# Kernel tuning notes

Hardware: AMD Instinct MI355X
Metric: run time of the kernel (lower is better)

Reference implementation:

```python
import jax, jax.numpy as jnp
import numpy as np

EPS = 1e-5
NUM_HEADS = 8
TOP_K = 4

def _ln(x, s, b):
    m = x.mean(-1, keepdims=True)
    v = ((x - m) ** 2).mean(-1, keepdims=True)
    return (x - m) / jnp.sqrt(v + EPS) * s + b

def _mha(x, wq, bq, wk, bk, wv, bv, wo, bo):
    B, S, D = x.shape
    dh = D // NUM_HEADS
    q = (x @ wq + bq).reshape(B, S, NUM_HEADS, dh)
    k = (x @ wk + bk).reshape(B, S, NUM_HEADS, dh)
    v = (x @ wv + bv).reshape(B, S, NUM_HEADS, dh)
    att = jnp.einsum('bqhd,bkhd->bhqk', q, k) / np.sqrt(dh).astype(x.dtype)
    a = jax.nn.softmax(att, axis=-1)
    o = jnp.einsum('bhqk,bkhd->bqhd', a, v).reshape(B, S, D)
    return o @ wo + bo

def _moe(x, rd, ru, w1, b1, w2, b2, ws1, bs1, ws2, bs2):
    B, S, D = x.shape
    N = B * S
    E = ru.shape[-1]
    t = x.reshape(N, D)
    scores = (t @ rd) @ ru                       # [N,E] low-rank router
    probs = jax.nn.softmax(scores, axis=-1)
    tv, ti = jax.lax.top_k(probs, TOP_K)          # [N,K]
    tw = tv / tv.sum(-1, keepdims=True)           # renormalized gate weights
    oh = jax.nn.one_hot(ti, E, dtype=t.dtype)     # [N,K,E]
    gates = (oh * tw[..., None]).sum(1)           # sparse [N,E] combine weights
    h = jax.nn.gelu(jnp.einsum('nd,edh->enh', t, w1) + b1[:, None, :])
    eo = jnp.einsum('enh,ehd->end', h, w2) + b2[:, None, :]
    routed = jnp.einsum('end,ne->nd', eo, gates)
    shared = jax.nn.gelu(t @ ws1 + bs1) @ ws2 + bs2
    out = (routed + shared).reshape(B, S, D)
    # aux losses: load-balance + router z-loss
    f = oh.sum(1).mean(0)                         # mean assignments per expert
    P = probs.mean(0)
    lb = (E / TOP_K) * jnp.sum(f * P)
    z = jnp.mean(jax.nn.logsumexp(scores, axis=-1) ** 2)
    return out, lb, z

def reference(x, ln1_s, ln1_b, ln2_s, ln2_b, wq, bq, wk, bk, wv, bv, wo, bo,
              router_down, router_up, w1, b1, w2, b2, ws1, bs1, ws2, bs2, fn_s, fn_b):
    L = wq.shape[0]
    lbs, zs = [], []
    for l in range(L):
        x = x + _mha(_ln(x, ln1_s[l], ln1_b[l]), wq[l], bq[l], wk[l], bk[l],
                     wv[l], bv[l], wo[l], bo[l])
        moe_out, lb, z = _moe(_ln(x, ln2_s[l], ln2_b[l]), router_down[l], router_up[l],
                              w1[l], b1[l], w2[l], b2[l], ws1[l], bs1[l], ws2[l], bs2[l])
        x = x + moe_out
        lbs.append(lb)
        zs.append(z)
    x = _ln(x, fn_s, fn_b)
    return x, jnp.stack(lbs), jnp.stack(zs)

def setup_inputs() -> dict:
    key = jax.random.key(0)
    ks = jax.random.split(key, 16)
    L, D, E, R, H, HS, B, S = 2, 512, 32, 64, 512, 4096, 4, 1024
    w = 0.02  # init scale for weights
    return {
        'x': jax.random.normal(ks[0], (B, S, D), jnp.float32),
        'ln1_s': jnp.ones((L, D)), 'ln1_b': jnp.zeros((L, D)),
        'ln2_s': jnp.ones((L, D)), 'ln2_b': jnp.zeros((L, D)),
        'wq': jax.random.normal(ks[1], (L, D, D)) * w, 'bq': jnp.zeros((L, D)),
        'wk': jax.random.normal(ks[2], (L, D, D)) * w, 'bk': jnp.zeros((L, D)),
        'wv': jax.random.normal(ks[3], (L, D, D)) * w, 'bv': jnp.zeros((L, D)),
        'wo': jax.random.normal(ks[4], (L, D, D)) * w, 'bo': jnp.zeros((L, D)),
        'router_down': jax.random.normal(ks[5], (L, D, R)) * w,
        'router_up': jax.random.normal(ks[6], (L, R, E)) * w,
        'w1': jax.random.normal(ks[7], (L, E, D, H)) * w, 'b1': jnp.zeros((L, E, H)),
        'w2': jax.random.normal(ks[8], (L, E, H, D)) * w, 'b2': jnp.zeros((L, E, D)),
        'ws1': jax.random.normal(ks[9], (L, D, HS)) * w, 'bs1': jnp.zeros((L, HS)),
        'ws2': jax.random.normal(ks[10], (L, HS, D)) * w, 'bs2': jnp.zeros((L, D)),
        'fn_s': jnp.ones((D,)), 'fn_b': jnp.zeros((D,)),
    }
```

## Files before the change

### kernel.cpp

```cpp
#include <hip/hip_runtime.h>
#include <math.h>

#define NTOK    4096
#define DMODEL  512
#define NEXP    32
#define RRANK   64
#define HEXP    512
#define HSHARED 4096
#define SEQ     1024
#define BATCH   4
#define NHEAD   8
#define TOPK    4
#define NLAYER  2
#define QBLK    64
#define KBLK    64
#define MAXTILE 160
#define DDU     262144

typedef __attribute__((ext_vector_type(8))) short bf16x8;
typedef __attribute__((ext_vector_type(4))) float f32x4;

__device__ __forceinline__ float gelu_f(float x) {
    float t = tanhf(0.7978845608028654f * (x + 0.044715f * x * x * x));
    return 0.5f * x * (1.f + t);
}
__device__ __forceinline__ unsigned short f2bf(float f) {
    unsigned int u = __float_as_uint(f);
    u += 0x7FFFu + ((u >> 16) & 1u);
    return (unsigned short)(u >> 16);
}
__device__ __forceinline__ float bf2f(unsigned short u) {
    return __uint_as_float((unsigned int)u << 16);
}
__device__ __forceinline__ void gl_lds16(const void* g, void* l) {
    __builtin_amdgcn_global_load_lds(
        (const __attribute__((address_space(1))) void*)g,
        (__attribute__((address_space(3))) void*)l, 16, 0, 0);
}

template <int MODE>
__global__ __launch_bounds__(256) void ln_kernel(const float* __restrict__ x,
                                                 const float* __restrict__ s,
                                                 const float* __restrict__ b,
                                                 float* __restrict__ outf,
                                                 unsigned short* __restrict__ outb) {
    int wave = threadIdx.x >> 6, lane = threadIdx.x & 63;
    int row = blockIdx.x * 4 + wave;
    const float* xr = x + (size_t)row * DMODEL;
    float v[8];
    float sum = 0.f;
#pragma unroll
    for (int i = 0; i < 8; i++) { v[i] = xr[lane + i * 64]; sum += v[i]; }
#pragma unroll
    for (int o = 32; o; o >>= 1) sum += __shfl_xor(sum, o);
    float m = sum * (1.f / DMODEL);
    float vs = 0.f;
#pragma unroll
    for (int i = 0; i < 8; i++) { float d = v[i] - m; vs += d * d; }
#pragma unroll
    for (int o = 32; o; o >>= 1) vs += __shfl_xor(vs, o);
    float rstd = rsqrtf(vs * (1.f / DMODEL) + 1e-5f);
#pragma unroll
    for (int i = 0; i < 8; i++) {
        int c = lane + i * 64;
        float r = (v[i] - m) * rstd * s[c] + b[c];
        if (MODE != 1) outf[(size_t)row * DMODEL + c] = r;
        if (MODE != 0) outb[(size_t)row * DMODEL + c] = f2bf(r);
    }
}

template <int SK, bool MOE, int MODE, bool ROUTER = false>
__global__ __launch_bounds__(256) void reduceln_kernel(
    const float* __restrict__ pbuf, const float* __restrict__ bias,
    const unsigned short* __restrict__ eogb, const float* __restrict__ topw,
    const int* __restrict__ pos, float* __restrict__ xb,
    const float* __restrict__ s, const float* __restrict__ b,
    float* __restrict__ outf, unsigned short* __restrict__ outb,
    const float* __restrict__ rdru, float* __restrict__ rsc) {
    int wave = threadIdx.x >> 6, lane = threadIdx.x & 63;
    int row = blockIdx.x * 4 + wave;
    int cb = lane * 8;
    size_t base = (size_t)row * DMODEL + cb;
    float v[8];
    {
        float4 a0 = *(const float4*)(xb + base);
        float4 a1 = *(const float4*)(xb + base + 4);
        float4 b0 = *(const float4*)(bias + cb);
        float4 b1 = *(const float4*)(bias + cb + 4);
        v[0] = a0.x + b0.x; v[1] = a0.y + b0.y; v[2] = a0.z + b0.z; v[3] = a0.w + b0.w;
        v[4] = a1.x + b1.x; v[5] = a1.y + b1.y; v[6] = a1.z + b1.z; v[7] = a1.w + b1.w;
    }
#pragma unroll
    for (int sk = 0; sk < SK; sk++) {
        const float* p = pbuf + (size_t)sk * NTOK * DMODEL + base;
        float4 p0 = *(const float4*)p;
        float4 p1 = *(const float4*)(p + 4);
        v[0] += p0.x; v[1] += p0.y; v[2] += p0.z; v[3] += p0.w;
        v[4] += p1.x; v[5] += p1.y; v[6] += p1.z; v[7] += p1.w;
    }
    if (MOE) {
#pragma unroll
        for (int k = 0; k < TOPK; k++) {
            float w = topw[row * TOPK + k];
            bf16x8 e = *(const bf16x8*)(eogb + (size_t)pos[row * TOPK + k] * DMODEL + cb);
#pragma unroll
            for (int i = 0; i < 8; i++) v[i] += w * bf2f((unsigned short)e[i]);
        }
    }
    *(float4*)(xb + base) = make_float4(v[0], v[1], v[2], v[3]);
    *(float4*)(xb + base + 4) = make_float4(v[4], v[5], v[6], v[7]);
    float sum = 0.f;
#pragma unroll
    for (int i = 0; i < 8; i++) sum += v[i];
#pragma unroll
    for (int o = 32; o; o >>= 1) sum += __shfl_xor(sum, o);
    float m = sum * (1.f / DMODEL);
    float vs = 0.f;
#pragma unroll
    for (int i = 0; i < 8; i++) { float d = v[i] - m; vs += d * d; }
#pragma unroll
    for (int o = 32; o; o >>= 1) vs += __shfl_xor(vs, o);
    float rstd = rsqrtf(vs * (1.f / DMODEL) + 1e-5f);
    float rr[8];
#pragma unroll
    for (int i = 0; i < 8; i++) {
        int c = cb + i;
        rr[i] = (v[i] - m) * rstd * s[c] + b[c];
        if (MODE != 1) outf[(size_t)row * DMODEL + c] = rr[i];
        if (MODE != 0) outb[(size_t)row * DMODEL + c] = f2bf(rr[i]);
    }
    if (ROUTER) {
        float sc[NEXP];
#pragma unroll
        for (int e = 0; e < NEXP; e++) sc[e] = 0.f;
#pragma unroll
        for (int i = 0; i < 8; i++) {
            const float4* rp = (const float4*)(rdru + (size_t)(cb + i) * NEXP);
            float rv = rr[i];
#pragma unroll
            for (int e4 = 0; e4 < 8; e4++) {
                float4 q = rp[e4];
                sc[e4 * 4 + 0] += rv * q.x;
                sc[e4 * 4 + 1] += rv * q.y;
                sc[e4 * 4 + 2] += rv * q.z;
                sc[e4 * 4 + 3] += rv * q.w;
            }
        }
#pragma unroll
        for (int e = 0; e < NEXP; e++) {
#pragma unroll
            for (int o = 32; o; o >>= 1) sc[e] += __shfl_xor(sc[e], o);
        }
        if (lane == 0) {
            float* rp = rsc + (size_t)row * NEXP;
#pragma unroll
            for (int e = 0; e < NEXP; e++) rp[e] = sc[e];
        }
    }
}

__global__ __launch_bounds__(256) void wtall_kernel(
    const float* __restrict__ wq, const float* __restrict__ wk,
    const float* __restrict__ wv, const float* __restrict__ wo,
    const float* __restrict__ w1, const float* __restrict__ w2,
    const float* __restrict__ ws1, const float* __restrict__ ws2,
    const float* __restrict__ bq, const float* __restrict__ bk, const float* __restrict__ bv,
    unsigned short* __restrict__ wqkvt, unsigned short* __restrict__ wot,
    unsigned short* __restrict__ w1t, unsigned short* __restrict__ w2t,
    unsigned short* __restrict__ ws1t, unsigned short* __restrict__ ws2t,
    float* __restrict__ bqkv, int* __restrict__ stats) {
    __shared__ float tbuf[64][68];
    int bkid = blockIdx.x;
    int tid = threadIdx.x;
    if (bkid >= 5376) {
        int i = (bkid - 5376) * 256 + tid;
        float val = (i < 512) ? bq[i] : (i < 1024 ? bk[i - 512] : bv[i - 1024]);
        bqkv[i] = val;
        if (i < 160) stats[i] = 0;
        return;
    }
    const float* src;
    unsigned short* dst;
    int K, N, tx, ty;
    if (bkid < 256) {
        int w = bkid >> 6, t = bkid & 63;
        K = 512; N = 512; ty = t >> 3; tx = t & 7;
        if (w == 0)      { src = wq; dst = wqkvt; }
        else if (w == 1) { src = wk; dst = wqkvt + DDU; }
        else if (w == 2) { src = wv; dst = wqkvt + 2 * (size_t)DDU; }
        else             { src = wo; dst = wot; }
    } else if (bkid < 2304) {
        int t = bkid - 256; int e = t >> 6; int tt = t & 63;
        K = 512; N = 512; ty = tt >> 3; tx = tt & 7;
        src = w1 + (size_t)e * DDU; dst = w1t + (size_t)e * DDU;
    } else if (bkid < 4352) {
        int t = bkid - 2304; int e = t >> 6; int tt = t & 63;
        K = 512; N = 512; ty = tt >> 3; tx = tt & 7;
        src = w2 + (size_t)e * DDU; dst = w2t + (size_t)e * DDU;
    } else if (bkid < 4864) {
        int t = bkid - 4352;
        K = 512; N = 4096; tx = t & 63; ty = t >> 6;
        src = ws1; dst = ws1t;
    } else {
        int t = bkid - 4864;
        K = 4096; N = 512; tx = t & 7; ty = t >> 3;
        src = ws2; dst = ws2t;
    }
    int k0 = ty * 64, n0 = tx * 64;
    int r = tid >> 2, cb4 = (tid & 3) * 4;
#pragma unroll
    for (int i = 0; i < 4; i++)
        *(float4*)&tbuf[r][cb4 + i * 16] = *(const float4*)(src + (size_t)(k0 + r) * N + n0 + cb4 + i * 16);
    __syncthreads();
    int g = tid & 7, nr = tid >> 3;
#pragma unroll
    for (int i = 0; i < 2; i++) {
        int n = nr + i * 32;
        bf16x8 v;
#pragma unroll
        for (int j = 0; j < 8; j++) v[j] = (short)f2bf(tbuf[g * 8 + j][n]);
        *(bf16x8*)(dst + (size_t)(n0 + n) * K + k0 + g * 8) = v;
    }
}

__global__ __launch_bounds__(256) void vtr_kernel(const unsigned short* __restrict__ QKV,
                                                  unsigned short* __restrict__ Vt) {
    int st = blockIdx.x, hh = blockIdx.y, bb = blockIdx.z;
    __shared__ unsigned short t[64][72];
    int r = threadIdx.x >> 3, g = threadIdx.x & 7;
#pragma unroll
    for (int i = 0; i < 2; i++) {
        int row = r + i * 32;
        bf16x8 v = *(const bf16x8*)(QKV + (size_t)(bb * SEQ + st * 64 + row) * 1536 + 1024 + hh * 64 + g * 8);
        *(bf16x8*)&t[row][g * 8] = v;
    }
    __syncthreads();
#pragma unroll
    for (int i = 0; i < 2; i++) {
        int d = r + i * 32;
        bf16x8 v;
#pragma unroll
        for (int j = 0; j < 8; j++) v[j] = (short)t[g * 8 + j][d];
        *(bf16x8*)(Vt + (size_t)((bb * NHEAD + hh) * 64 + d) * SEQ + st * 64 + g * 8) = v;
    }
}

template <bool GELU, bool GATHER, bool EXPERT, bool OUTBF16, int SK>
__device__ __forceinline__ void gemm_body(
    char* asb, char* bsb,
    unsigned int rb, unsigned int gx, unsigned int tot, int zidx,
    const unsigned short* Ab, const unsigned short* Wt,
    const float* bias, void* Cvoid, int M, int Nn, int Kk,
    const int* rowmap, const int* cntp, const int* offp, const int* tinfo) {
    constexpr int RS  = 128;
    constexpr int CH  = 8;
    constexpr int RPI = 8;
    constexpr int AIW = 4;
    constexpr int BIW = 2;
    unsigned int lg = (rb & 7) * (tot >> 3) + (rb >> 3);
    unsigned int bx = lg % gx;
    unsigned int by = lg / gx;
    int n0 = bx * 64;
    int m0;
    size_t cbase = 0;
    int kbeg = 0, kend = Kk;
    if (EXPERT) {
        int t = by;
        if (t >= tinfo[0]) return;
        int e = tinfo[1 + 2 * t];
        m0 = tinfo[2 + 2 * t];
        M = cntp[e];
        Wt += (size_t)e * Nn * Kk;
        bias += (size_t)e * Nn;
        int oe = offp[e];
        cbase = (size_t)oe * Nn;
        if (GATHER) rowmap += oe;
        else Ab += (size_t)oe * Kk;
    } else {
        m0 = by * 128;
    }
    if (SK > 1) {
        int chunk = Kk / SK;
        kbeg = zidx * chunk;
        kend = kbeg + chunk;
        cbase = (size_t)zidx * M * Nn;
    }
    int tid = threadIdx.x;
    int wave = tid >> 6, lane = tid & 63;
    int wm = wave >> 1, wn = wave & 1;
    int l15 = lane & 15, l16 = lane >> 4;
    int c16 = lane & (CH - 1);
    int ro  = lane / CH;

    const char* aptr[AIW];
    const char* bptr[BIW];
#pragma unroll
    for (int j = 0; j < AIW; j++) {
        int rloc = j * RPI + ro;
        int row = wave * 32 + rloc;
        int grow = m0 + row;
        int arow = GATHER ? rowmap[grow] : grow;
        int srcoff = ((c16 ^ (rloc & (CH - 1))) << 4);
        aptr[j] = (const char*)Ab + (((size_t)arow * Kk) << 1) + srcoff;
    }
#pragma unroll
    for (int j = 0; j < BIW; j++) {
        int rloc = j * RPI + ro;
        int row = wave * 16 + rloc;
        int srcoff = ((c16 ^ (rloc & (CH - 1))) << 4);
        bptr[j] = (const char*)Wt + (((size_t)(n0 + row) * Kk) << 1) + srcoff;
    }

    f32x4 acc[4][2];
#pragma unroll
    for (int m = 0; m < 4; m++)
#pragma unroll
        for (int n = 0; n < 2; n++)
#pragma unroll
            for (int j = 0; j < 4; j++) acc[m][n][j] = 0.f;

    for (int k0 = kbeg; k0 < kend; k0 += 64) {
        size_t kb = (size_t)k0 << 1;
#pragma unroll
        for (int j = 0; j < AIW; j++) gl_lds16(aptr[j] + kb, asb + wave * 32 * RS + j * 1024);
#pragma unroll
        for (int j = 0; j < BIW; j++) gl_lds16(bptr[j] + kb, bsb + wave * 16 * RS + j * 1024);
        __syncthreads();
#pragma unroll
        for (int kk = 0; kk < 2; kk++) {
            int k8 = kk * 4 + l16;
            bf16x8 a[4], b[2];
#pragma unroll
            for (int m = 0; m < 4; m++) {
                int row = wm * 64 + m * 16 + l15;
                a[m] = *(const bf16x8*)(asb + row * RS + ((k8 * 16) ^ ((row & (CH - 1)) << 4)));
            }
#pragma unroll
            for (int n = 0; n < 2; n++) {
                int row = wn * 32 + n * 16 + l15;
                b[n] = *(const bf16x8*)(bsb + row * RS + ((k8 * 16) ^ ((row & (CH - 1)) << 4)));
            }
#pragma unroll
            for (int m = 0; m < 4; m++)
#pragma unroll
                for (int n = 0; n < 2; n++)
                    acc[m][n] = __builtin_amdgcn_mfma_f32_16x16x32_bf16(a[m], b[n], acc[m][n], 0, 0, 0);
        }
        __syncthreads();
    }

#pragma unroll
    for (int m = 0; m < 4; m++) {
#pragma unroll
        for (int n = 0; n < 2; n++) {
            int col = n0 + wn * 32 + n * 16 + l15;
            float bv = (SK == 1 && bias) ? bias[col] : 0.f;
#pragma unroll
            for (int j = 0; j < 4; j++) {
                int row = m0 + wm * 64 + m * 16 + l16 * 4 + j;
                if (row >= M) continue;
                float val = acc[m][n][j] + bv;
                if (SK == 1 && GELU) val = gelu_f(val);
                if (SK == 1 && OUTBF16)
                    ((unsigned short*)Cvoid)[cbase + (size_t)row * Nn + col] = f2bf(val);
                else
                    ((float*)Cvoid)[cbase + (size_t)row * Nn + col] = val;
            }
        }
    }
}

template <bool GELU, bool GATHER, bool EXPERT, bool OUTBF16, int SK = 1>
__global__ __launch_bounds__(256, 2) void gemm_mfma(
    const unsigned short* __restrict__ Ab, const unsigned short* __restrict__ Wt,
    const float* __restrict__ bias, void* __restrict__ Cvoid,
    int M, int Nn, int Kk,
    const int* __restrict__ rowmap, const int* __restrict__ cntp,
    const int* __restrict__ offp, const int* __restrict__ tinfo) {
    __shared__ short As[128 * 64];
    __shared__ short Bs[64 * 64];
    gemm_body<GELU, GATHER, EXPERT, OUTBF16, SK>(
        (char*)As, (char*)Bs,
        blockIdx.y * gridDim.x + blockIdx.x, gridDim.x, gridDim.x * gridDim.y, blockIdx.z,
        Ab, Wt, bias, Cvoid, M, Nn, Kk, rowmap, cntp, offp, tinfo);
}

__global__ __launch_bounds__(256, 2) void mlp1_kernel(
    const unsigned short* __restrict__ hb,
    const unsigned short* __restrict__ ws1t, const float* __restrict__ bs1,
    unsigned short* __restrict__ hidb,
    const unsigned short* __restrict__ w1t, const float* __restrict__ b1,
    unsigned short* __restrict__ ehid,
    const int* __restrict__ perm, const int* __restrict__ cnt,
    const int* __restrict__ poff, const int* __restrict__ tinfo) {
    __shared__ short As[128 * 64];
    __shared__ short Bs[64 * 64];
    unsigned int bid = blockIdx.x;
    if (bid < 2048) {
        gemm_body<true, false, false, true, 1>(
            (char*)As, (char*)Bs, bid, 64, 2048, 0,
            hb, ws1t, bs1, hidb, NTOK, HSHARED, DMODEL, nullptr, nullptr, nullptr, nullptr);
    } else {
        gemm_body<true, true, true, true, 1>(
            (char*)As, (char*)Bs, bid - 2048, 8, 1280, 0,
            hb, w1t, b1, ehid, 0, HEXP, DMODEL, perm, cnt, poff, tinfo);
    }
}

__global__ __launch_bounds__(256, 2) void mlp2_kernel(
    const unsigned short* __restrict__ hidb,
    const unsigned short* __restrict__ ws2t, float* __restrict__ pbuf,
    const unsigned short* __restrict__ ehid,
    const unsigned short* __restrict__ w2t, const float* __restrict__ b2,
    unsigned short* __restrict__ eogb,
    const int* __restrict__ cnt, const int* __restrict__ poff,
    const int* __restrict__ tinfo) {
    __shared__ short As[128 * 64];
    __shared__ short Bs[64 * 64];
    unsigned int bid = blockIdx.x;
    if (bid < 1024) {
        int zidx = bid >> 8;
        gemm_body<false, false, false, false, 4>(
            (char*)As, (char*)Bs, bid & 255, 8, 256, zidx,
            hidb, ws2t, nullptr, pbuf, NTOK, DMODEL, HSHARED, nullptr, nullptr, nullptr, nullptr);
    } else {
        gemm_body<false, false, true, true, 1>(
            (char*)As, (char*)Bs, bid - 1024, 8, 1280, 0,
            ehid, w2t, b2, eogb, 0, DMODEL, HEXP, nullptr, cnt, poff, tinfo);
    }
}

template <bool GELU>
__global__ __launch_bounds__(256) void gemm_tile(
    const float* __restrict__ A, const float* __restrict__ W,
    float* __restrict__ C, int M, int Nn, int Kk, int lda) {
    int n0 = blockIdx.x * 64;
    int m0 = blockIdx.y * 64;
    __shared__ float Asf[16][68];
    __shared__ float Wsf[16][68];
    int tid = threadIdx.x;
    int ml = tid >> 2, kl = (tid & 3) << 2;
    bool avalid = (m0 + ml) < M;
    int arow = m0 + ml;
    const float* aptr = A + (size_t)arow * lda + kl;
    int kr = tid >> 4, nc = (tid & 15) << 2;
    bool wvalid = (n0 + nc) < Nn;
    const float* wptr = W + (size_t)kr * Nn + n0 + nc;
    int tm = (tid >> 4) << 2, tn = (tid & 15) << 2;
    float acc[4][4] = {{0.f}};
    for (int k0 = 0; k0 < Kk; k0 += 16) {
        float4 av = make_float4(0.f, 0.f, 0.f, 0.f);
        float4 wv = make_float4(0.f, 0.f, 0.f, 0.f);
        if (avalid) av = *(const float4*)(aptr + k0);
        if (wvalid) wv = *(const float4*)(wptr + (size_t)k0 * Nn);
        Asf[kl + 0][ml] = av.x; Asf[kl + 1][ml] = av.y;
        Asf[kl + 2][ml] = av.z; Asf[kl + 3][ml] = av.w;
        *(float4*)&Wsf[kr][nc] = wv;
        __syncthreads();
#pragma unroll
        for (int kk = 0; kk < 16; kk++) {
            float4 a4 = *(const float4*)&Asf[kk][tm];
            float4 w4 = *(const float4*)&Wsf[kk][tn];
            acc[0][0] += a4.x * w4.x; acc[0][1] += a4.x * w4.y; acc[0][2] += a4.x * w4.z; acc[0][3] += a4.x * w4.w;
            acc[1][0] += a4.y * w4.x; acc[1][1] += a4.y * w4.y; acc[1][2] += a4.y * w4.z; acc[1][3] += a4.y * w4.w;
            acc[2][0] += a4.z * w4.x; acc[2][1] += a4.z * w4.y; acc[2][2] += a4.z * w4.z; acc[2][3] += a4.z * w4.w;
            acc[3][0] += a4.w * w4.x; acc[3][1] += a4.w * w4.y; acc[3][2] += a4.w * w4.z; acc[3][3] += a4.w * w4.w;
        }
        __syncthreads();
    }
#pragma unroll
    for (int i = 0; i < 4; i++) {
        int mm = m0 + tm + i;
        if (mm >= M) break;
        float* crow = C + (size_t)mm * Nn;
#pragma unroll
        for (int j = 0; j < 4; j++) {
            int nn = n0 + tn + j;
            if (nn >= Nn) continue;
            float val = acc[i][j];
            if (GELU) val = gelu_f(val);
            crow[nn] = val;
        }
    }
}

__global__ __launch_bounds__(256, 2) void attn_mfma(const unsigned short* __restrict__ QKV,
                                                    const unsigned short* __restrict__ Vt,
                                                    unsigned short* __restrict__ O) {
    int qt = blockIdx.x, hh = blockIdx.y, bb = blockIdx.z;
    __shared__ char lds[32768];
    char* Qs = lds;
    char* Ks = lds + 8192;
    char* Vs = lds + 16384;
    char* Ps = lds + 24576;
    int tid = threadIdx.x;
    int w = tid >> 6, l = tid & 63;
    int l15 = l & 15, l16 = l >> 4;

    {
        int r = tid >> 3, g = tid & 7;
        const unsigned short* qbase = QKV + (size_t)(bb * SEQ + qt * QBLK) * 1536 + hh * 64;
#pragma unroll
        for (int i = 0; i < 2; i++) {
            int row = r + i * 32;
            bf16x8 v = *(const bf16x8*)(qbase + (size_t)row * 1536 + g * 8);
            *(bf16x8*)(Qs + row * 128 + ((g * 16) ^ ((row & 7) << 4))) = v;
        }
    }
    f32x4 accO[4];
#pragma unroll
    for (int n = 0; n < 4; n++)
#pragma unroll
        for (int j = 0; j < 4; j++) accO[n][j] = 0.f;
    float m_r[4] = {-1e30f, -1e30f, -1e30f, -1e30f};
    float l_r[4] = {0.f, 0.f, 0.f, 0.f};

    const unsigned short* kbase = QKV + (size_t)(bb * SEQ) * 1536 + 512 + hh * 64;
    const unsigned short* vbase = Vt + (size_t)((bb * NHEAD + hh) * 64) * SEQ;

    for (int kt = 0; kt < SEQ / KBLK; kt++) {
        __syncthreads();
        {
            int r = tid >> 3, g = tid & 7;
#pragma unroll
            for (int i = 0; i < 2; i++) {
                int row = r + i * 32;
                bf16x8 kv = *(const bf16x8*)(kbase + (size_t)(kt * KBLK + row) * 1536 + g * 8);
                *(bf16x8*)(Ks + row * 128 + ((g * 16) ^ ((row & 7) << 4))) = kv;
                bf16x8 vv = *(const bf16x8*)(vbase + (size_t)row * SEQ + kt * KBLK + g * 8);
                *(bf16x8*)(Vs + row * 128 + ((g * 16) ^ ((row & 7) << 4))) = vv;
            }
        }
        __syncthreads();
        f32x4 s_acc[4];
#pragma unroll
        for (int n = 0; n < 4; n++)
#pragma unroll
            for (int j = 0; j < 4; j++) s_acc[n][j] = 0.f;
#pragma unroll
        for (int st = 0; st < 2; st++) {
            int kb = st * 64 + l16 * 16;
            int qrow = w * 16 + l15;
            bf16x8 a = *(const bf16x8*)(Qs + qrow * 128 + (kb ^ ((qrow & 7) << 4)));
#pragma unroll
            for (int n = 0; n < 4; n++) {
                int kr = n * 16 + l15;
                bf16x8 b = *(const bf16x8*)(Ks + kr * 128 + (kb ^ ((kr & 7) << 4)));
                s_acc[n] = __builtin_amdgcn_mfma_f32_16x16x32_bf16(a, b, s_acc[n], 0, 0, 0);
            }
        }
        char* pw = Ps + w * 2048;
#pragma unroll
        for (int j = 0; j < 4; j++) {
            float s0 = s_acc[0][j] * 0.125f, s1 = s_acc[1][j] * 0.125f;
            float s2 = s_acc[2][j] * 0.125f, s3 = s_acc[3][j] * 0.125f;
            float tmax = fmaxf(fmaxf(s0, s1), fmaxf(s2, s3));
#pragma unroll
            for (int o = 1; o < 16; o <<= 1) tmax = fmaxf(tmax, __shfl_xor(tmax, o));
            float mnew = fmaxf(m_r[j], tmax);
            float resc = __expf(m_r[j] - mnew);
            float p0 = __expf(s0 - mnew), p1 = __expf(s1 - mnew);
            float p2 = __expf(s2 - mnew), p3 = __expf(s3 - mnew);
            float ps = p0 + p1 + p2 + p3;
#pragma unroll
            for (int o = 1; o < 16; o <<= 1) ps += __shfl_xor(ps, o);
            l_r[j] = l_r[j] * resc + ps;
            m_r[j] = mnew;
            accO[0][j] *= resc; accO[1][j] *= resc;
            accO[2][j] *= resc; accO[3][j] *= resc;
            int prow = l16 * 4 + j;
            int sw = (prow & 7) << 4;
            *(unsigned short*)(pw + prow * 128 + ((2 * l15) ^ sw)) = f2bf(p0);
            *(unsigned short*)(pw + prow * 128 + ((2 * l15 + 32) ^ sw)) = f2bf(p1);
            *(unsigned short*)(pw + prow * 128 + ((2 * l15 + 64) ^ sw)) = f2bf(p2);
            *(unsigned short*)(pw + prow * 128 + ((2 * l15 + 96) ^ sw)) = f2bf(p3);
        }
#pragma unroll
        for (int st = 0; st < 2; st++) {
            int kb = st * 64 + l16 * 16;
            bf16x8 pa = *(const bf16x8*)(pw + l15 * 128 + (kb ^ ((l15 & 7) << 4)));
#pragma unroll
            for (int n = 0; n < 4; n++) {
                int vr = n * 16 + l15;
                bf16x8 vb = *(const bf16x8*)(Vs + vr * 128 + (kb ^ ((vr & 7) << 4)));
                accO[n] = __builtin_amdgcn_mfma_f32_16x16x32_bf16(pa, vb, accO[n], 0, 0, 0);
            }
        }
    }
    unsigned short* obase = O + (size_t)(bb * SEQ + qt * QBLK + w * 16) * DMODEL + hh * 64;
#pragma unroll
    for (int j = 0; j < 4; j++) {
        float inv = 1.f / l_r[j];
        int row = l16 * 4 + j;
#pragma unroll
        for (int n = 0; n < 4; n++)
            obase[(size_t)row * DMODEL + n * 16 + l15] = f2bf(accO[n][j] * inv);
    }
}

__global__ __launch_bounds__(256) void router_topk(const float* __restrict__ rsc,
                                                   float* __restrict__ topw,
                                                   int* __restrict__ topi,
                                                   int* __restrict__ cnt,
                                                   float* __restrict__ sumP,
                                                   float* __restrict__ zacc) {
    __shared__ float wP[4][NEXP];
    __shared__ int wC[4][NEXP];
    __shared__ float wZ[4];
    int tid = threadIdx.x;
    int wv = tid >> 6, lane = tid & 63;
    int n = blockIdx.x * 256 + tid;
    float sc[NEXP];
    float mx = -1e30f;
#pragma unroll
    for (int e = 0; e < NEXP; e++) { sc[e] = rsc[n * NEXP + e]; mx = fmaxf(mx, sc[e]); }
    float se = 0.f;
#pragma unroll
    for (int e = 0; e < NEXP; e++) { sc[e] = expf(sc[e] - mx); se += sc[e]; }
    float invse = 1.f / se;
    float lse = mx + logf(se);
    float z = lse * lse;
#pragma unroll
    for (int o = 32; o; o >>= 1) z += __shfl_xor(z, o);
    if (lane == 0) wZ[wv] = z;
#pragma unroll
    for (int e = 0; e < NEXP; e++) {
        float pv = sc[e] * invse;
#pragma unroll
        for (int o = 32; o; o >>= 1) pv += __shfl_xor(pv, o);
        if (lane == 0) wP[wv][e] = pv;
    }
    float tv[TOPK]; int ti[TOPK];
#pragma unroll
    for (int k = 0; k < TOPK; k++) {
        float best = -1.f; int bi = 0;
#pragma unroll
        for (int e = 0; e < NEXP; e++) {
            if (sc[e] > best) { best = sc[e]; bi = e; }
        }
        tv[k] = best * invse; ti[k] = bi; sc[bi] = -1.f;
    }
    float s4 = tv[0] + tv[1] + tv[2] + tv[3];
#pragma unroll
    for (int k = 0; k < TOPK; k++) {
        topw[n * TOPK + k] = tv[k] / s4;
        topi[n * TOPK + k] = ti[k];
    }
#pragma unroll
    for (int e = 0; e < NEXP; e++) {
        unsigned long long b0 = __ballot(ti[0] == e);
        unsigned long long b1 = __ballot(ti[1] == e);
        unsigned long long b2 = __ballot(ti[2] == e);
        unsigned long long b3 = __ballot(ti[3] == e);
        if (lane == 0)
            wC[wv][e] = __popcll(b0) + __popcll(b1) + __popcll(b2) + __popcll(b3);
    }
    __syncthreads();
    if (tid < NEXP) {
        atomicAdd(&sumP[tid], wP[0][tid] + wP[1][tid] + wP[2][tid] + wP[3][tid]);
        atomicAdd(&cnt[tid], wC[0][tid] + wC[1][tid] + wC[2][tid] + wC[3][tid]);
    }
    if (tid == 0) atomicAdd(zacc, wZ[0] + wZ[1] + wZ[2] + wZ[3]);
}

__global__ void scanaux_kernel(const int* __restrict__ cnt, int* __restrict__ poff,
                               int* __restrict__ tinfo, int* __restrict__ perm,
                               const float* __restrict__ sumP, const float* __restrict__ zacc,
                               float* __restrict__ out_aux, int l) {
    int lane = threadIdx.x;
    int c = (lane < NEXP) ? cnt[lane] : 0;
    int nt = (c + 127) >> 7;
    int x = nt;
#pragma unroll
    for (int o = 1; o < 32; o <<= 1) {
        int y = __shfl_up(x, o);
        if (lane >= o) x += y;
    }
    int excl = x - nt;
    if (lane < NEXP) {
        poff[lane] = excl * 128;
        for (int i = 0; i < nt; i++) {
            tinfo[1 + 2 * (excl + i)] = lane;
            tinfo[2 + 2 * (excl + i)] = i * 128;
        }
        for (int i = c; i < nt * 128; i++) perm[excl * 128 + i] = 0;
    }
    float lb = (lane < NEXP) ? ((float)c / (float)NTOK) * (sumP[lane] / (float)NTOK) : 0.f;
#pragma unroll
    for (int o = 32; o; o >>= 1) lb += __shfl_xor(lb, o);
    if (lane == 31) {
        tinfo[0] = x;
        out_aux[l] = lb * (float)NEXP / (float)TOPK;
        out_aux[NLAYER + l] = zacc[0] / (float)NTOK;
    }
}

__global__ __launch_bounds__(256) void scatter_kernel(const int* __restrict__ topi,
                                                      const int* __restrict__ poff,
                                                      int* __restrict__ cursor,
                                                      int* __restrict__ perm,
                                                      int* __restrict__ pos) {
    __shared__ int lcnt[NEXP];
    __shared__ int lbase[NEXP];
    if (threadIdx.x < NEXP) lcnt[threadIdx.x] = 0;
    __syncthreads();
    int i = blockIdx.x * 256 + threadIdx.x;
    int e = topi[i];
    int lr = atomicAdd(&lcnt[e], 1);
    __syncthreads();
    if (threadIdx.x < NEXP && lcnt[threadIdx.x] > 0)
        lbase[threadIdx.x] = atomicAdd(&cursor[threadIdx.x], lcnt[threadIdx.x]);
    __syncthreads();
    int g = poff[e] + lbase[e] + lr;
    perm[g] = i >> 2;
    pos[i] = g;
}

extern "C" void kernel_launch(void* const* d_in, const int* in_sizes, int n_in,
                              void* d_out, int out_size, void* d_ws, size_t ws_size,
                              hipStream_t stream) {
    (void)in_sizes; (void)n_in; (void)out_size; (void)ws_size;
    const float* x_in  = (const float*)d_in[0];
    const float* ln1_s = (const float*)d_in[1];
    const float* ln1_b = (const float*)d_in[2];
    const float* ln2_s = (const float*)d_in[3];
    const float* ln2_b = (const float*)d_in[4];
    const float* wq = (const float*)d_in[5];
    const float* bq = (const float*)d_in[6];
    const float* wk = (const float*)d_in[7];
    const float* bk = (const float*)d_in[8];
    const float* wv = (const float*)d_in[9];
    const float* bv = (const float*)d_in[10];
    const float* wo = (const float*)d_in[11];
    const float* bo = (const float*)d_in[12];
    const float* rdw = (const float*)d_in[13];
    const float* ruw = (const float*)d_in[14];
    const float* w1 = (const float*)d_in[15];
    const float* b1 = (const float*)d_in[16];
    const float* w2 = (const float*)d_in[17];
    const float* b2 = (const float*)d_in[18];
    const float* ws1 = (const float*)d_in[19];
    const float* bs1 = (const float*)d_in[20];
    const float* ws2 = (const float*)d_in[21];
    const float* bs2 = (const float*)d_in[22];
    const float* fn_s = (const float*)d_in[23];
    const float* fn_b = (const float*)d_in[24];

    float* ws = (float*)d_ws;
    const size_t ND = (size_t)NTOK * DMODEL;
    const size_t PADROWS = (size_t)MAXTILE * 128;
    size_t o = 0;
    float* xb  = ws + o; o += ND;
    unsigned short* hb     = (unsigned short*)(ws + o); o += ND / 2;
    unsigned short* qkv_bf = (unsigned short*)(ws + o); o += (size_t)NTOK * 1536 / 2;
    unsigned short* vT     = (unsigned short*)(ws + o); o += ND / 2;
    unsigned short* t1b    = (unsigned short*)(ws + o); o += ND / 2;
    unsigned short* hidb   = (unsigned short*)(ws + o); o += (size_t)NTOK * HSHARED / 2;
    unsigned short* ehid   = (unsigned short*)(ws + o); o += PADROWS * HEXP / 2;
    unsigned short* eogb   = (unsigned short*)(ws + o); o += PADROWS * DMODEL / 2;
    float* pbuf = ws + o; o += 4 * ND;
    float* rdru = ws + o; o += (size_t)DMODEL * NEXP;
    float* rsc  = ws + o; o += (size_t)NTOK * NEXP;
    float* topw = ws + o; o += (size_t)NTOK * TOPK;
    float* bqkv = ws + o; o += 1536;
    int* topi = (int*)(ws + o); o += (size_t)NTOK * TOPK;
    int* pos  = (int*)(ws + o); o += (size_t)NTOK * TOPK;
    int* perm = (int*)(ws + o); o += PADROWS;
    int* stats = (int*)(ws + o); o += 256;
    int* tinfo = (int*)(ws + o); o += 512;
    int* cnt = stats;
    int* cursor = stats + 32;
    int* poff = stats + 64;
    float* sumP = (float*)(stats + 96);
    float* zacc = sumP + 32;
    unsigned short* wbf = (unsigned short*)(ws + o);
    unsigned short* wqkvt = wbf;
    unsigned short* wot  = wqkvt + 3 * (size_t)DDU;
    unsigned short* w1t  = wot + DDU;
    unsigned short* w2t  = w1t + (size_t)NEXP * DDU;
    unsigned short* ws1t = w2t + (size_t)NEXP * DDU;
    unsigned short* ws2t = ws1t + (size_t)DMODEL * HSHARED;

    float* out_x = (float*)d_out;
    float* out_aux = out_x + ND;

    hipMemcpyAsync(xb, x_in, ND * sizeof(float), hipMemcpyDeviceToDevice, stream);

    dim3 blk(256);
    dim3 gQKV(1536 / 64, NTOK / 128);
    dim3 gOP(DMODEL / 64, NTOK / 128, 2);

    for (int l = 0; l < NLAYER; l++) {
        const size_t DD = (size_t)DMODEL * DMODEL;
        wtall_kernel<<<5382, blk, 0, stream>>>(
            wq + l * DD, wk + l * DD, wv + l * DD, wo + l * DD,
            w1 + (size_t)l * NEXP * DD, w2 + (size_t)l * NEXP * DD,
            ws1 + (size_t)l * DMODEL * HSHARED, ws2 + (size_t)l * HSHARED * DMODEL,
            bq + l * DMODEL, bk + l * DMODEL, bv + l * DMODEL,
            wqkvt, wot, w1t, w2t, ws1t, ws2t, bqkv, stats);
        gemm_tile<false><<<dim3(1, 8), blk, 0, stream>>>(
            rdw + (size_t)l * DMODEL * RRANK, ruw + (size_t)l * RRANK * NEXP, rdru, DMODEL, NEXP, RRANK, RRANK);

        if (l == 0)
            ln_kernel<1><<<NTOK / 4, blk, 0, stream>>>(xb, ln1_s, ln1_b, nullptr, hb);
        gemm_mfma<false, false, false, true><<<gQKV, blk, 0, stream>>>(
            hb, wqkvt, bqkv, qkv_bf, NTOK, 1536, DMODEL, nullptr, nullptr, nullptr, nullptr);
        vtr_kernel<<<dim3(SEQ / 64, NHEAD, BATCH), blk, 0, stream>>>(qkv_bf, vT);
        attn_mfma<<<dim3(SEQ / QBLK, NHEAD, BATCH), blk, 0, stream>>>(qkv_bf, vT, t1b);
        gemm_mfma<false, false, false, false, 2><<<gOP, blk, 0, stream>>>(
            t1b, wot, nullptr, pbuf, NTOK, DMODEL, DMODEL, nullptr, nullptr, nullptr, nullptr);
        reduceln_kernel<2, false, 1, true><<<NTOK / 4, blk, 0, stream>>>(
            pbuf, bo + l * DMODEL, nullptr, nullptr, nullptr, xb,
            ln2_s + l * DMODEL, ln2_b + l * DMODEL, nullptr, hb, rdru, rsc);
        router_topk<<<NTOK / 256, blk, 0, stream>>>(rsc, topw, topi, cnt, sumP, zacc);
        scanaux_kernel<<<1, 64, 0, stream>>>(cnt, poff, tinfo, perm, sumP, zacc, out_aux, l);
        scatter_kernel<<<NTOK * TOPK / 256, blk, 0, stream>>>(topi, poff, cursor, perm, pos);
        mlp1_kernel<<<3328, blk, 0, stream>>>(
            hb, ws1t, bs1 + (size_t)l * HSHARED, hidb,
            w1t, b1 + (size_t)l * NEXP * HEXP, ehid,
            perm, cnt, poff, tinfo);
        mlp2_kernel<<<2304, blk, 0, stream>>>(
            hidb, ws2t, pbuf,
            ehid, w2t, b2 + (size_t)l * NEXP * DMODEL, eogb,
            cnt, poff, tinfo);
        if (l + 1 < NLAYER) {
            reduceln_kernel<4, true, 1, false><<<NTOK / 4, blk, 0, stream>>>(
                pbuf, bs2 + l * DMODEL, eogb, topw, pos, xb,
                ln1_s + (l + 1) * DMODEL, ln1_b + (l + 1) * DMODEL, nullptr, hb, nullptr, nullptr);
        } else {
            reduceln_kernel<4, true, 0, false><<<NTOK / 4, blk, 0, stream>>>(
                pbuf, bs2 + l * DMODEL, eogb, topw, pos, xb,
                fn_s, fn_b, out_x, nullptr, nullptr, nullptr);
        }
    }
}
```

Before: 533.2 us.

## Overlap next-layer weight transposes with current-layer GEMM kernels

Only layer 0 keeps the standalone weight-transpose pass and the router-matrix GEMM. For later layers, the fp32-to-bf16 transposes, bias packing, stats reset and rdru product are split across extra blocks appended to the previous layer's QKV, MLP1 and MLP2 kernels. The goal is to drop a large memory-bound launch from the critical path by letting it fill idle compute units alongside the GEMMs. The cost is larger grids, a heavier mixed workload per launch, and tighter buffer-lifetime ordering between layers.

```diff
diff --git a/kernel.cpp b/kernel.cpp
--- a/kernel.cpp
+++ b/kernel.cpp
@@ -159,6 +159,70 @@
     }
 }
 
+__device__ __forceinline__ void wt_tile_body(char* ldsraw, const float* src,
+                                             unsigned short* dst, int K, int N,
+                                             int tx, int ty) {
+    float (*tbuf)[68] = (float(*)[68])ldsraw;
+    int tid = threadIdx.x;
+    int k0 = ty * 64, n0 = tx * 64;
+    int r = tid >> 2, cb4 = (tid & 3) * 4;
+#pragma unroll
+    for (int i = 0; i < 4; i++)
+        *(float4*)&tbuf[r][cb4 + i * 16] = *(const float4*)(src + (size_t)(k0 + r) * N + n0 + cb4 + i * 16);
+    __syncthreads();
+    int g = tid & 7, nr = tid >> 3;
+#pragma unroll
+    for (int i = 0; i < 2; i++) {
+        int n = nr + i * 32;
+        bf16x8 v;
+#pragma unroll
+        for (int j = 0; j < 8; j++) v[j] = (short)f2bf(tbuf[g * 8 + j][n]);
+        *(bf16x8*)(dst + (size_t)(n0 + n) * K + k0 + g * 8) = v;
+    }
+}
+
+__device__ __forceinline__ void rdru_tile_body(char* ldsraw, const float* A,
+                                               const float* W, float* C, int m0) {
+    float (*Asf)[68] = (float(*)[68])ldsraw;
+    float (*Wsf)[68] = (float(*)[68])(ldsraw + 4352);
+    int tid = threadIdx.x;
+    int ml = tid >> 2, kl = (tid & 3) << 2;
+    const float* aptr = A + (size_t)(m0 + ml) * RRANK + kl;
+    int kr = tid >> 4, nc = (tid & 15) << 2;
+    bool wvalid = nc < NEXP;
+    const float* wptr = W + (size_t)kr * NEXP + nc;
+    int tm = (tid >> 4) << 2, tn = (tid & 15) << 2;
+    float acc[4][4] = {{0.f}};
+    for (int k0 = 0; k0 < RRANK; k0 += 16) {
+        float4 av = *(const float4*)(aptr + k0);
+        float4 wv = make_float4(0.f, 0.f, 0.f, 0.f);
+        if (wvalid) wv = *(const float4*)(wptr + (size_t)k0 * NEXP);
+        Asf[kl + 0][ml] = av.x; Asf[kl + 1][ml] = av.y;
+        Asf[kl + 2][ml] = av.z; Asf[kl + 3][ml] = av.w;
+        *(float4*)&Wsf[kr][nc] = wv;
+        __syncthreads();
+#pragma unroll
+        for (int kk = 0; kk < 16; kk++) {
+            float4 a4 = *(const float4*)&Asf[kk][tm];
+            float4 w4 = *(const float4*)&Wsf[kk][tn];
+            acc[0][0] += a4.x * w4.x; acc[0][1] += a4.x * w4.y; acc[0][2] += a4.x * w4.z; acc[0][3] += a4.x * w4.w;
+            acc[1][0] += a4.y * w4.x; acc[1][1] += a4.y * w4.y; acc[1][2] += a4.y * w4.z; acc[1][3] += a4.y * w4.w;
+            acc[2][0] += a4.z * w4.x; acc[2][1] += a4.z * w4.y; acc[2][2] += a4.z * w4.z; acc[2][3] += a4.z * w4.w;
+            acc[3][0] += a4.w * w4.x; acc[3][1] += a4.w * w4.y; acc[3][2] += a4.w * w4.z; acc[3][3] += a4.w * w4.w;
+        }
+        __syncthreads();
+    }
+#pragma unroll
+    for (int i = 0; i < 4; i++) {
+        float* crow = C + (size_t)(m0 + tm + i) * NEXP;
+#pragma unroll
+        for (int j = 0; j < 4; j++) {
+            int nn = tn + j;
+            if (nn < NEXP) crow[nn] = acc[i][j];
+        }
+    }
+}
+
 __global__ __launch_bounds__(256) void wtall_kernel(
     const float* __restrict__ wq, const float* __restrict__ wk,
     const float* __restrict__ wv, const float* __restrict__ wo,
@@ -169,7 +233,7 @@
     unsigned short* __restrict__ w1t, unsigned short* __restrict__ w2t,
     unsigned short* __restrict__ ws1t, unsigned short* __restrict__ ws2t,
     float* __restrict__ bqkv, int* __restrict__ stats) {
-    __shared__ float tbuf[64][68];
+    __shared__ char lds[24576];
     int bkid = blockIdx.x;
     int tid = threadIdx.x;
     if (bkid >= 5376) {
@@ -206,21 +270,7 @@
         K = 4096; N = 512; tx = t & 7; ty = t >> 3;
         src = ws2; dst = ws2t;
     }
-    int k0 = ty * 64, n0 = tx * 64;
-    int r = tid >> 2, cb4 = (tid & 3) * 4;
-#pragma unroll
-    for (int i = 0; i < 4; i++)
-        *(float4*)&tbuf[r][cb4 + i * 16] = *(const float4*)(src + (size_t)(k0 + r) * N + n0 + cb4 + i * 16);
-    __syncthreads();
-    int g = tid & 7, nr = tid >> 3;
-#pragma unroll
-    for (int i = 0; i < 2; i++) {
-        int n = nr + i * 32;
-        bf16x8 v;
-#pragma unroll
-        for (int j = 0; j < 8; j++) v[j] = (short)f2bf(tbuf[g * 8 + j][n]);
-        *(bf16x8*)(dst + (size_t)(n0 + n) * K + k0 + g * 8) = v;
-    }
+    wt_tile_body(lds, src, dst, K, N, tx, ty);
 }
 
 __global__ __launch_bounds__(256) void vtr_kernel(const unsigned short* __restrict__ QKV,
@@ -377,12 +427,38 @@
     int M, int Nn, int Kk,
     const int* __restrict__ rowmap, const int* __restrict__ cntp,
     const int* __restrict__ offp, const int* __restrict__ tinfo) {
-    __shared__ short As[128 * 64];
-    __shared__ short Bs[64 * 64];
+    __shared__ char lds[24576];
     gemm_body<GELU, GATHER, EXPERT, OUTBF16, SK>(
-        (char*)As, (char*)Bs,
+        lds, lds + 16384,
         blockIdx.y * gridDim.x + blockIdx.x, gridDim.x, gridDim.x * gridDim.y, blockIdx.z,
         Ab, Wt, bias, Cvoid, M, Nn, Kk, rowmap, cntp, offp, tinfo);
+}
+
+__global__ __launch_bounds__(256, 2) void qkv_kernel(
+    const unsigned short* __restrict__ hb, const unsigned short* __restrict__ wqkvt,
+    const float* __restrict__ bqkv, unsigned short* __restrict__ qkv_bf,
+    const float* __restrict__ w2src, const float* __restrict__ ws2src,
+    unsigned short* __restrict__ w2t, unsigned short* __restrict__ ws2t,
+    int* __restrict__ stats) {
+    __shared__ char lds[24576];
+    unsigned int bid = blockIdx.x;
+    if (bid < 768) {
+        gemm_body<false, false, false, true, 1>(
+            lds, lds + 16384, bid, 24, 768, 0,
+            hb, wqkvt, bqkv, qkv_bf, NTOK, 1536, DMODEL, nullptr, nullptr, nullptr, nullptr);
+    } else {
+        unsigned int eb = bid - 768;
+        if (eb < 2048) {
+            int e = eb >> 6, tt = eb & 63;
+            wt_tile_body(lds, w2src + (size_t)e * DDU, w2t + (size_t)e * DDU,
+                         512, 512, tt & 7, tt >> 3);
+        } else if (eb < 2560) {
+            int t = eb - 2048;
+            wt_tile_body(lds, ws2src, ws2t, 4096, 512, t & 7, t >> 3);
+        } else {
+            if (threadIdx.x < 160) stats[threadIdx.x] = 0;
+        }
+    }
 }
 
 __global__ __launch_bounds__(256, 2) void mlp1_kernel(
@@ -392,18 +468,40 @@
     const unsigned short* __restrict__ w1t, const float* __restrict__ b1,
     unsigned short* __restrict__ ehid,
     const int* __restrict__ perm, const int* __restrict__ cnt,
-    const int* __restrict__ poff, const int* __restrict__ tinfo) {
-    __shared__ short As[128 * 64];
-    __shared__ short Bs[64 * 64];
+    const int* __restrict__ poff, const int* __restrict__ tinfo,
+    const float* __restrict__ nwq, const float* __restrict__ nwk,
+    const float* __restrict__ nwv, const float* __restrict__ nwo,
+    const float* __restrict__ nbq, const float* __restrict__ nbk, const float* __restrict__ nbv,
+    unsigned short* __restrict__ wqkvt, unsigned short* __restrict__ wot,
+    float* __restrict__ bqkv,
+    const float* __restrict__ nrdw, const float* __restrict__ nruw, float* __restrict__ rdru) {
+    __shared__ char lds[24576];
     unsigned int bid = blockIdx.x;
     if (bid < 2048) {
         gemm_body<true, false, false, true, 1>(
-            (char*)As, (char*)Bs, bid, 64, 2048, 0,
+            lds, lds + 16384, bid, 64, 2048, 0,
             hb, ws1t, bs1, hidb, NTOK, HSHARED, DMODEL, nullptr, nullptr, nullptr, nullptr);
+    } else if (bid < 3328) {
+        gemm_body<true, true, true, true, 1>(
+            lds, lds + 16384, bid - 2048, 8, 1280, 0,
+            hb, w1t, b1, ehid, 0, HEXP, DMODEL, perm, cnt, poff, tinfo);
     } else {
-        gemm_body<true, true, true, true, 1>(
-            (char*)As, (char*)Bs, bid - 2048, 8, 1280, 0,
-            hb, w1t, b1, ehid, 0, HEXP, DMODEL, perm, cnt, poff, tinfo);
+        unsigned int eb = bid - 3328;
+        if (eb < 256) {
+            int w = eb >> 6, t = eb & 63;
+            const float* src; unsigned short* dst;
+            if (w == 0)      { src = nwq; dst = wqkvt; }
+            else if (w == 1) { src = nwk; dst = wqkvt + DDU; }
+            else if (w == 2) { src = nwv; dst = wqkvt + 2 * (size_t)DDU; }
+            else             { src = nwo; dst = wot; }
+            wt_tile_body(lds, src, dst, 512, 512, t & 7, t >> 3);
+        } else if (eb < 262) {
+            int i = (eb - 256) * 256 + threadIdx.x;
+            float val = (i < 512) ? nbq[i] : (i < 1024 ? nbk[i - 512] : nbv[i - 1024]);
+            bqkv[i] = val;
+        } else {
+            rdru_tile_body(lds, nrdw, nruw, rdru, (eb - 262) * 64);
+        }
     }
 }
 
@@ -414,74 +512,38 @@
     const unsigned short* __restrict__ w2t, const float* __restrict__ b2,
     unsigned short* __restrict__ eogb,
     const int* __restrict__ cnt, const int* __restrict__ poff,
-    const int* __restrict__ tinfo) {
-    __shared__ short As[128 * 64];
-    __shared__ short Bs[64 * 64];
+    const int* __restrict__ tinfo,
+    const float* __restrict__ nw1, const float* __restrict__ nws1,
+    unsigned short* __restrict__ w1t, unsigned short* __restrict__ ws1t) {
+    __shared__ char lds[24576];
     unsigned int bid = blockIdx.x;
     if (bid < 1024) {
         int zidx = bid >> 8;
         gemm_body<false, false, false, false, 4>(
-            (char*)As, (char*)Bs, bid & 255, 8, 256, zidx,
+            lds, lds + 16384, bid & 255, 8, 256, zidx,
             hidb, ws2t, nullptr, pbuf, NTOK, DMODEL, HSHARED, nullptr, nullptr, nullptr, nullptr);
+    } else if (bid < 2304) {
+        gemm_body<false, false, true, true, 1>(
+            lds, lds + 16384, bid - 1024, 8, 1280, 0,
+            ehid, w2t, b2, eogb, 0, DMODEL, HEXP, nullptr, cnt, poff, tinfo);
     } else {
-        gemm_body<false, false, true, true, 1>(
-            (char*)As, (char*)Bs, bid - 1024, 8, 1280, 0,
-            ehid, w2t, b2, eogb, 0, DMODEL, HEXP, nullptr, cnt, poff, tinfo);
-    }
-}
-
-template <bool GELU>
+        unsigned int eb = bid - 2304;
+        if (eb < 2048) {
+            int e = eb >> 6, tt = eb & 63;
+            wt_tile_body(lds, nw1 + (size_t)e * DDU, w1t + (size_t)e * DDU,
+                         512, 512, tt & 7, tt >> 3);
+        } else {
+            int t = eb - 2048;
+            wt_tile_body(lds, nws1, ws1t, 512, 4096, t & 63, t >> 6);
+        }
+    }
+}
+
 __global__ __launch_bounds__(256) void gemm_tile(
     const float* __restrict__ A, const float* __restrict__ W,
-    float* __restrict__ C, int M, int Nn, int Kk, int lda) {
-    int n0 = blockIdx.x * 64;
-    int m0 = blockIdx.y * 64;
-    __shared__ float Asf[16][68];
-    __shared__ float Wsf[16][68];
-    int tid = threadIdx.x;
-    int ml = tid >> 2, kl = (tid & 3) << 2;
-    bool avalid = (m0 + ml) < M;
-    int arow = m0 + ml;
-    const float* aptr = A + (size_t)arow * lda + kl;
-    int kr = tid >> 4, nc = (tid & 15) << 2;
-    bool wvalid = (n0 + nc) < Nn;
-    const float* wptr = W + (size_t)kr * Nn + n0 + nc;
-    int tm = (tid >> 4) << 2, tn = (tid & 15) << 2;
-    float acc[4][4] = {{0.f}};
-    for (int k0 = 0; k0 < Kk; k0 += 16) {
-        float4 av = make_float4(0.f, 0.f, 0.f, 0.f);
-        float4 wv = make_float4(0.f, 0.f, 0.f, 0.f);
-        if (avalid) av = *(const float4*)(aptr + k0);
-        if (wvalid) wv = *(const float4*)(wptr + (size_t)k0 * Nn);
-        Asf[kl + 0][ml] = av.x; Asf[kl + 1][ml] = av.y;
-        Asf[kl + 2][ml] = av.z; Asf[kl + 3][ml] = av.w;
-        *(float4*)&Wsf[kr][nc] = wv;
-        __syncthreads();
-#pragma unroll
-        for (int kk = 0; kk < 16; kk++) {
-            float4 a4 = *(const float4*)&Asf[kk][tm];
-            float4 w4 = *(const float4*)&Wsf[kk][tn];
-            acc[0][0] += a4.x * w4.x; acc[0][1] += a4.x * w4.y; acc[0][2] += a4.x * w4.z; acc[0][3] += a4.x * w4.w;
-            acc[1][0] += a4.y * w4.x; acc[1][1] += a4.y * w4.y; acc[1][2] += a4.y * w4.z; acc[1][3] += a4.y * w4.w;
-            acc[2][0] += a4.z * w4.x; acc[2][1] += a4.z * w4.y; acc[2][2] += a4.z * w4.z; acc[2][3] += a4.z * w4.w;
-            acc[3][0] += a4.w * w4.x; acc[3][1] += a4.w * w4.y; acc[3][2] += a4.w * w4.z; acc[3][3] += a4.w * w4.w;
-        }
-        __syncthreads();
-    }
-#pragma unroll
-    for (int i = 0; i < 4; i++) {
-        int mm = m0 + tm + i;
-        if (mm >= M) break;
-        float* crow = C + (size_t)mm * Nn;
-#pragma unroll
-        for (int j = 0; j < 4; j++) {
-            int nn = n0 + tn + j;
-            if (nn >= Nn) continue;
-            float val = acc[i][j];
-            if (GELU) val = gelu_f(val);
-            crow[nn] = val;
-        }
-    }
+    float* __restrict__ C) {
+    __shared__ char lds[16384];
+    rdru_tile_body(lds, A, W, C, blockIdx.x * 64);
 }
 
 __global__ __launch_bounds__(256, 2) void attn_mfma(const unsigned short* __restrict__ QKV,
@@ -787,24 +849,27 @@
     hipMemcpyAsync(xb, x_in, ND * sizeof(float), hipMemcpyDeviceToDevice, stream);
 
     dim3 blk(256);
-    dim3 gQKV(1536 / 64, NTOK / 128);
     dim3 gOP(DMODEL / 64, NTOK / 128, 2);
 
     for (int l = 0; l < NLAYER; l++) {
         const size_t DD = (size_t)DMODEL * DMODEL;
-        wtall_kernel<<<5382, blk, 0, stream>>>(
-            wq + l * DD, wk + l * DD, wv + l * DD, wo + l * DD,
-            w1 + (size_t)l * NEXP * DD, w2 + (size_t)l * NEXP * DD,
-            ws1 + (size_t)l * DMODEL * HSHARED, ws2 + (size_t)l * HSHARED * DMODEL,
-            bq + l * DMODEL, bk + l * DMODEL, bv + l * DMODEL,
-            wqkvt, wot, w1t, w2t, ws1t, ws2t, bqkv, stats);
-        gemm_tile<false><<<dim3(1, 8), blk, 0, stream>>>(
-            rdw + (size_t)l * DMODEL * RRANK, ruw + (size_t)l * RRANK * NEXP, rdru, DMODEL, NEXP, RRANK, RRANK);
-
-        if (l == 0)
+        if (l == 0) {
+            wtall_kernel<<<5382, blk, 0, stream>>>(
+                wq, wk, wv, wo, w1, w2, ws1, ws2,
+                bq, bk, bv,
+                wqkvt, wot, w1t, w2t, ws1t, ws2t, bqkv, stats);
+            gemm_tile<<<8, blk, 0, stream>>>(rdw, ruw, rdru);
             ln_kernel<1><<<NTOK / 4, blk, 0, stream>>>(xb, ln1_s, ln1_b, nullptr, hb);
-        gemm_mfma<false, false, false, true><<<gQKV, blk, 0, stream>>>(
-            hb, wqkvt, bqkv, qkv_bf, NTOK, 1536, DMODEL, nullptr, nullptr, nullptr, nullptr);
+        }
+        if (l == 0) {
+            qkv_kernel<<<768, blk, 0, stream>>>(
+                hb, wqkvt, bqkv, qkv_bf, nullptr, nullptr, nullptr, nullptr, nullptr);
+        } else {
+            qkv_kernel<<<3329, blk, 0, stream>>>(
+                hb, wqkvt, bqkv, qkv_bf,
+                w2 + (size_t)l * NEXP * DD, ws2 + (size_t)l * HSHARED * DMODEL,
+                w2t, ws2t, stats);
+        }
         vtr_kernel<<<dim3(SEQ / 64, NHEAD, BATCH), blk, 0, stream>>>(qkv_bf, vT);
         attn_mfma<<<dim3(SEQ / QBLK, NHEAD, BATCH), blk, 0, stream>>>(qkv_bf, vT, t1b);
         gemm_mfma<false, false, false, false, 2><<<gOP, blk, 0, stream>>>(
@@ -815,15 +880,26 @@
         router_topk<<<NTOK / 256, blk, 0, stream>>>(rsc, topw, topi, cnt, sumP, zacc);
         scanaux_kernel<<<1, 64, 0, stream>>>(cnt, poff, tinfo, perm, sumP, zacc, out_aux, l);
         scatter_kernel<<<NTOK * TOPK / 256, blk, 0, stream>>>(topi, poff, cursor, perm, pos);
-        mlp1_kernel<<<3328, blk, 0, stream>>>(
+        bool hasNext = (l + 1 < NLAYER);
+        int ln1g = hasNext ? 3598 : 3328;
+        int lnx = hasNext ? (l + 1) : l;
+        mlp1_kernel<<<ln1g, blk, 0, stream>>>(
             hb, ws1t, bs1 + (size_t)l * HSHARED, hidb,
             w1t, b1 + (size_t)l * NEXP * HEXP, ehid,
-            perm, cnt, poff, tinfo);
-        mlp2_kernel<<<2304, blk, 0, stream>>>(
+            perm, cnt, poff, tinfo,
+            wq + (size_t)lnx * DD, wk + (size_t)lnx * DD,
+            wv + (size_t)lnx * DD, wo + (size_t)lnx * DD,
+            bq + (size_t)lnx * DMODEL, bk + (size_t)lnx * DMODEL, bv + (size_t)lnx * DMODEL,
+            wqkvt, wot, bqkv,
+            rdw + (size_t)lnx * DMODEL * RRANK, ruw + (size_t)lnx * RRANK * NEXP, rdru);
+        int ln2g = hasNext ? 4864 : 2304;
+        mlp2_kernel<<<ln2g, blk, 0, stream>>>(
             hidb, ws2t, pbuf,
             ehid, w2t, b2 + (size_t)l * NEXP * DMODEL, eogb,
-            cnt, poff, tinfo);
-        if (l + 1 < NLAYER) {
+            cnt, poff, tinfo,
+            w1 + (size_t)lnx * NEXP * DD, ws1 + (size_t)lnx * DMODEL * HSHARED,
+            w1t, ws1t);
+        if (hasNext) {
             reduceln_kernel<4, true, 1, false><<<NTOK / 4, blk, 0, stream>>>(
                 pbuf, bs2 + l * DMODEL, eogb, topw, pos, xb,
                 ln1_s + (l + 1) * DMODEL, ln1_b + (l + 1) * DMODEL, nullptr, hb, nullptr, nullptr);
```

After: 521.9 us. 2.1% less time.
